# Performance work log

Hardware: AMD Instinct MI355X
Metric: run time of the kernel (lower is better)

## Reference

```python
import jax, jax.numpy as jnp
import numpy as np

D = 2048      # hidden_size
H = 16        # num_attention_heads
KVH = 4       # num_key_value_heads
HD = 128      # head_dim
E = 32        # num_experts
TOPK = 8      # num_experts_per_tok
F = 768       # moe_intermediate_size
EPS = 1e-6
THETA = 1000000.0
B, S = 2, 1024


def setup_inputs() -> dict:
    key = jax.random.key(0)
    ks = jax.random.split(key, 16)
    sc = lambda *shape: 1.0 / np.sqrt(shape[-2] if len(shape) > 1 else shape[0])
    return {
        "hidden_states": jax.random.normal(ks[0], (B, S, D), jnp.float32),
        "attention_mask": jnp.ones((B, S), jnp.bool_),
        "input_ln_scale": jnp.ones((D,), jnp.float32),
        "post_ln_scale": jnp.ones((D,), jnp.float32),
        "q_w": jax.random.normal(ks[1], (D, H * HD), jnp.float32) * sc(D, H * HD),
        "k_w": jax.random.normal(ks[2], (D, KVH * HD), jnp.float32) * sc(D, KVH * HD),
        "v_w": jax.random.normal(ks[3], (D, KVH * HD), jnp.float32) * sc(D, KVH * HD),
        "o_w": jax.random.normal(ks[4], (H * HD, D), jnp.float32) * sc(H * HD, D),
        "q_norm_scale": jnp.ones((HD,), jnp.float32),
        "k_norm_scale": jnp.ones((HD,), jnp.float32),
        "gate_w": jax.random.normal(ks[5], (D, E), jnp.float32) * sc(D, E),
        "gate_proj": jax.random.normal(ks[6], (E, D, F), jnp.float32) * sc(E, D, F),
        "up_proj": jax.random.normal(ks[7], (E, D, F), jnp.float32) * sc(E, D, F),
        "down_proj": jax.random.normal(ks[8], (E, F, D), jnp.float32) * sc(E, F, D),
    }


def _rms(x, scale):
    return x * jax.lax.rsqrt(jnp.mean(x * x, axis=-1, keepdims=True) + EPS) * scale


def _rope(x):
    # x: [B, S, h, HD]
    half = HD // 2
    inv_freq = 1.0 / (THETA ** (jnp.arange(0, half, dtype=jnp.float32) / half))
    freqs = jnp.arange(x.shape[1], dtype=jnp.float32)[:, None] * inv_freq  # [S, HD/2]
    cos = jnp.concatenate([jnp.cos(freqs)] * 2, axis=-1)[None, :, None, :]
    sin = jnp.concatenate([jnp.sin(freqs)] * 2, axis=-1)[None, :, None, :]
    rot = jnp.concatenate([-x[..., half:], x[..., :half]], axis=-1)
    return x * cos + rot * sin


def _forward(hidden_states, attention_mask, input_ln_scale, post_ln_scale,
             q_w, k_w, v_w, o_w, q_norm_scale, k_norm_scale,
             gate_w, gate_proj, up_proj, down_proj):
    b, s, _ = hidden_states.shape
    residual = hidden_states
    h = _rms(hidden_states, input_ln_scale)

    # ---- Qwen3 attention (GQA + per-head RMSNorm + RoPE, causal) ----
    q = _rms((h @ q_w).reshape(b, s, H, HD), q_norm_scale)
    k = _rms((h @ k_w).reshape(b, s, KVH, HD), k_norm_scale)
    v = (h @ v_w).reshape(b, s, KVH, HD)
    q, k = _rope(q), _rope(k)
    rep = H // KVH
    k = jnp.repeat(k, rep, axis=2)  # [B,S,H,HD]
    v = jnp.repeat(v, rep, axis=2)
    scores = jnp.einsum('bqhd,bkhd->bhqk', q, k) * (HD ** -0.5)
    causal = jnp.tril(jnp.ones((s, s), jnp.bool_))
    mask = causal[None, None] & attention_mask[:, None, None, :]
    scores = jnp.where(mask, scores, jnp.finfo(scores.dtype).min)
    attn = jax.nn.softmax(scores, axis=-1)
    ctx = jnp.einsum('bhqk,bkhd->bqhd', attn, v).reshape(b, s, H * HD)
    h = residual + ctx @ o_w

    # ---- MoE block ----
    residual = h
    x = _rms(h, post_ln_scale).reshape(-1, D)  # [N, D]
    router_logits = x @ gate_w                 # [N, E]
    routing_weights, selected = jax.lax.top_k(router_logits, k=TOPK)
    routing_weights = jax.nn.softmax(routing_weights, axis=-1)
    sel_flat = jnp.ravel(selected)                     # [N*K]
    x_exp = jnp.repeat(x, TOPK, axis=0)                # [N*K, D]
    sort_idx = jnp.argsort(sel_flat)
    unsort_idx = jnp.argsort(sort_idx)
    x_sorted = x_exp[sort_idx]
    group_sizes = jnp.bincount(sel_flat, length=E)
    gate_out = jax.lax.ragged_dot(x_sorted, gate_proj, group_sizes)
    up_out = jax.lax.ragged_dot(x_sorted, up_proj, group_sizes)
    activated = jax.nn.silu(gate_out) * up_out
    down_out = jax.lax.ragged_dot(activated, down_proj, group_sizes)
    unsorted = down_out[unsort_idx].reshape(-1, TOPK, D)
    moe_out = (unsorted * routing_weights[..., None]).sum(axis=1).reshape(b, s, D)
    return residual + moe_out


def reference(hidden_states, attention_mask, input_ln_scale, post_ln_scale,
              q_w, k_w, v_w, o_w, q_norm_scale, k_norm_scale,
              gate_w, gate_proj, up_proj, down_proj):
    return _forward(hidden_states, attention_mask, input_ln_scale, post_ln_scale,
                    q_w, k_w, v_w, o_w, q_norm_scale, k_norm_scale,
                    gate_w, gate_proj, up_proj, down_proj)
```

## Files before the change

### kernel.cpp

```cpp
#include <hip/hip_runtime.h>
#include <hip/hip_bf16.h>

#define D_ 2048
#define H_ 16
#define KVH_ 4
#define HD_ 128
#define E_ 32
#define TOPK_ 8
#define F_ 768
#define NB_ 2
#define SS_ 1024
#define NT_ 2048
#define NPAIR_ 16384

typedef __attribute__((ext_vector_type(8))) short short8;
typedef __attribute__((ext_vector_type(4))) float floatx4;
typedef __attribute__((ext_vector_type(4))) unsigned int uintx4;
typedef __attribute__((ext_vector_type(4))) unsigned short ushortx4;

__device__ __forceinline__ unsigned short f2bf(float f) {
  union { float f; unsigned u; } v; v.f = f;
  unsigned r = v.u + 0x7FFFu + ((v.u >> 16) & 1u);
  return (unsigned short)(r >> 16);
}
__device__ __forceinline__ float bf2f(unsigned short h) {
  union { unsigned u; float f; } v; v.u = ((unsigned)h) << 16;
  return v.f;
}
__device__ __forceinline__ void split2(float v, unsigned short& hi, unsigned short& lo) {
  unsigned short h = f2bf(v);
  hi = h;
  lo = f2bf(v - bf2f(h));
}
__device__ __forceinline__ void gload16(const unsigned short* g, unsigned short* l) {
  __builtin_amdgcn_global_load_lds(
      (const __attribute__((address_space(1))) unsigned int*)g,
      (__attribute__((address_space(3))) unsigned int*)l, 16, 0, 0);
}

__global__ __launch_bounds__(256) void tconv_kernel(const float* __restrict__ src,
                                                    unsigned short* __restrict__ dst,
                                                    int R, int C) {
  size_t off = (size_t)blockIdx.z * R * C;
  src += off; dst += off;
  __shared__ float t[32][33];
  int c0 = blockIdx.x * 32, r0 = blockIdx.y * 32;
  int row = threadIdx.x >> 3, c4 = (threadIdx.x & 7) * 4;
  float4 v = *(const float4*)(src + (size_t)(r0 + row) * C + c0 + c4);
  t[row][c4 + 0] = v.x; t[row][c4 + 1] = v.y; t[row][c4 + 2] = v.z; t[row][c4 + 3] = v.w;
  __syncthreads();
  ushortx4 o = { f2bf(t[c4 + 0][row]), f2bf(t[c4 + 1][row]),
                 f2bf(t[c4 + 2][row]), f2bf(t[c4 + 3][row]) };
  *(ushortx4*)(dst + (size_t)(c0 + row) * R + r0 + c4) = o;
}

__global__ __launch_bounds__(256) void tsplit_kernel(const float* __restrict__ src,
                                                     unsigned short* __restrict__ dhi,
                                                     unsigned short* __restrict__ dlo,
                                                     int R, int C) {
  __shared__ float t[32][33];
  int c0 = blockIdx.x * 32, r0 = blockIdx.y * 32;
  int row = threadIdx.x >> 3, c4 = (threadIdx.x & 7) * 4;
  float4 v = *(const float4*)(src + (size_t)(r0 + row) * C + c0 + c4);
  t[row][c4 + 0] = v.x; t[row][c4 + 1] = v.y; t[row][c4 + 2] = v.z; t[row][c4 + 3] = v.w;
  __syncthreads();
  ushortx4 oh, ol;
  #pragma unroll
  for (int i = 0; i < 4; ++i) {
    unsigned short hi, lo;
    split2(t[c4 + i][row], hi, lo);
    oh[i] = hi; ol[i] = lo;
  }
  size_t didx = (size_t)(c0 + row) * R + r0 + c4;
  *(ushortx4*)(dhi + didx) = oh;
  *(ushortx4*)(dlo + didx) = ol;
}

template<int MODE>
__global__ __launch_bounds__(256) void rms_kernel(const float* __restrict__ in,
                                                  const float* __restrict__ sc,
                                                  float* __restrict__ outf,
                                                  unsigned short* __restrict__ o1,
                                                  unsigned short* __restrict__ o2) {
  __shared__ float red[4];
  int row = blockIdx.x, tid = threadIdx.x;
  const float4* x4 = (const float4*)(in + (size_t)row * D_);
  float4 a = x4[tid], b = x4[tid + 256];
  float ss = a.x*a.x + a.y*a.y + a.z*a.z + a.w*a.w
           + b.x*b.x + b.y*b.y + b.z*b.z + b.w*b.w;
  #pragma unroll
  for (int off = 1; off < 64; off <<= 1) ss += __shfl_xor(ss, off);
  if ((tid & 63) == 0) red[tid >> 6] = ss;
  __syncthreads();
  float r = rsqrtf((red[0] + red[1] + red[2] + red[3]) * (1.0f / D_) + 1e-6f);
  const float4* s4 = (const float4*)sc;
  float4 sa = s4[tid], sb = s4[tid + 256];
  float va[8] = { a.x*r*sa.x, a.y*r*sa.y, a.z*r*sa.z, a.w*r*sa.w,
                  b.x*r*sb.x, b.y*r*sb.y, b.z*r*sb.z, b.w*r*sb.w };
  if (MODE == 0) {
    ushortx4 h0, l0, h1, l1;
    #pragma unroll
    for (int i = 0; i < 4; ++i) { unsigned short h, l; split2(va[i], h, l); h0[i] = h; l0[i] = l; }
    #pragma unroll
    for (int i = 0; i < 4; ++i) { unsigned short h, l; split2(va[4 + i], h, l); h1[i] = h; l1[i] = l; }
    *(ushortx4*)(o1 + (size_t)row * D_ + tid * 4) = h0;
    *(ushortx4*)(o2 + (size_t)row * D_ + tid * 4) = l0;
    *(ushortx4*)(o1 + (size_t)row * D_ + 1024 + tid * 4) = h1;
    *(ushortx4*)(o2 + (size_t)row * D_ + 1024 + tid * 4) = l1;
  } else {
    *(float4*)(outf + (size_t)row * D_ + tid * 4) = make_float4(va[0], va[1], va[2], va[3]);
    *(float4*)(outf + (size_t)row * D_ + 1024 + tid * 4) = make_float4(va[4], va[5], va[6], va[7]);
    ushortx4 h0 = { f2bf(va[0]), f2bf(va[1]), f2bf(va[2]), f2bf(va[3]) };
    ushortx4 h1 = { f2bf(va[4]), f2bf(va[5]), f2bf(va[6]), f2bf(va[7]) };
    *(ushortx4*)(o1 + (size_t)row * D_ + tid * 4) = h0;
    *(ushortx4*)(o1 + (size_t)row * D_ + 1024 + tid * 4) = h1;
  }
}

template<int EPI>
__global__ __launch_bounds__(256) void gemm_bb(const unsigned short* __restrict__ Ahi,
                                               const unsigned short* __restrict__ Alo,
                                               const unsigned short* __restrict__ Bhi,
                                               const unsigned short* __restrict__ Blo,
                                               const float* __restrict__ res,
                                               float* __restrict__ out,
                                               int M, int Nn, int K) {
  __shared__ unsigned short Ah[64 * 72], Al[64 * 72], Bh[64 * 72], Bl[64 * 72];
  int tid = threadIdx.x, l = tid & 63, wid = tid >> 6;
  int lr = l & 15, lk = (l >> 4) * 8;
  int m0 = blockIdx.y * 64, n0 = blockIdx.x * 64;
  int wr = (wid >> 1) * 32, wc = (wid & 1) * 32;
  int srow = tid >> 3, sch = (tid & 7) * 8;
  size_t aoff[2], boff[2];
  int loff[2];
  #pragma unroll
  for (int i = 0; i < 2; ++i) {
    aoff[i] = (size_t)(m0 + i * 32 + srow) * K + sch;
    boff[i] = (size_t)(n0 + i * 32 + srow) * K + sch;
    loff[i] = (i * 32 + srow) * 72 + sch;
  }
  floatx4 acc[2][2];
  #pragma unroll
  for (int i = 0; i < 2; ++i)
    #pragma unroll
    for (int j = 0; j < 2; ++j) acc[i][j] = (floatx4){0.f, 0.f, 0.f, 0.f};
  for (int k0 = 0; k0 < K; k0 += 64) {
    uintx4 vah[2], val[2], vbh[2], vbl[2];
    #pragma unroll
    for (int i = 0; i < 2; ++i) {
      vah[i] = *(const uintx4*)(Ahi + aoff[i] + k0);
      val[i] = *(const uintx4*)(Alo + aoff[i] + k0);
      vbh[i] = *(const uintx4*)(Bhi + boff[i] + k0);
      vbl[i] = *(const uintx4*)(Blo + boff[i] + k0);
    }
    __syncthreads();
    #pragma unroll
    for (int i = 0; i < 2; ++i) {
      *(uintx4*)&Ah[loff[i]] = vah[i];
      *(uintx4*)&Al[loff[i]] = val[i];
      *(uintx4*)&Bh[loff[i]] = vbh[i];
      *(uintx4*)&Bl[loff[i]] = vbl[i];
    }
    __syncthreads();
    #pragma unroll
    for (int ks = 0; ks < 2; ++ks) {
      short8 ah[2], al_[2], bh[2], bl_[2];
      #pragma unroll
      for (int i = 0; i < 2; ++i) {
        ah[i]  = *(const short8*)&Ah[(wr + i * 16 + lr) * 72 + ks * 32 + lk];
        al_[i] = *(const short8*)&Al[(wr + i * 16 + lr) * 72 + ks * 32 + lk];
        bh[i]  = *(const short8*)&Bh[(wc + i * 16 + lr) * 72 + ks * 32 + lk];
        bl_[i] = *(const short8*)&Bl[(wc + i * 16 + lr) * 72 + ks * 32 + lk];
      }
      #pragma unroll
      for (int i = 0; i < 2; ++i)
        #pragma unroll
        for (int j = 0; j < 2; ++j) {
          acc[i][j] = __builtin_amdgcn_mfma_f32_16x16x32_bf16(ah[i], bh[j], acc[i][j], 0, 0, 0);
          acc[i][j] = __builtin_amdgcn_mfma_f32_16x16x32_bf16(ah[i], bl_[j], acc[i][j], 0, 0, 0);
          acc[i][j] = __builtin_amdgcn_mfma_f32_16x16x32_bf16(al_[i], bh[j], acc[i][j], 0, 0, 0);
        }
    }
  }
  int rq = (l >> 4) * 4;
  #pragma unroll
  for (int i = 0; i < 2; ++i)
    #pragma unroll
    for (int j = 0; j < 2; ++j)
      #pragma unroll
      for (int r = 0; r < 4; ++r) {
        size_t idx = (size_t)(m0 + wr + i * 16 + rq + r) * Nn + (n0 + wc + j * 16 + lr);
        float v = acc[i][j][r];
        if (EPI == 1) v += res[idx];
        out[idx] = v;
      }
}

template<int EPI>
__global__ __launch_bounds__(256) void gemm_bb128g(const unsigned short* __restrict__ Ahi,
                                                   const unsigned short* __restrict__ Alo,
                                                   const unsigned short* __restrict__ Bhi,
                                                   const unsigned short* __restrict__ Blo,
                                                   const float* __restrict__ res,
                                                   float* __restrict__ out,
                                                   int M, int Nn, int K) {
  int g = blockIdx.x;
  int nwg = gridDim.x;
  int per = nwg >> 3;
  int sw = (g & 7) * per + (g >> 3);
  int my = M >> 7;
  int xt = sw / my, yt = sw - xt * my;
  int m0 = yt * 128, n0 = xt * 128;
  __shared__ unsigned short Ah[2][128 * 32], Al[2][128 * 32];
  __shared__ unsigned short Bh[2][128 * 32], Bl[2][128 * 32];
  int tid = threadIdx.x, l = tid & 63, wid = tid >> 6;
  int lr = l & 15, lk = (l >> 4) * 8;
  int wr = (wid >> 1) * 64, wc = (wid & 1) * 64;
  int srl = l >> 2;
  int sch = ((l & 3) ^ (srl & 3)) * 8;
  size_t aoffs[2], boffs[2];
  int ldo[2];
  #pragma unroll
  for (int i = 0; i < 2; ++i) {
    int r = wid * 32 + i * 16 + srl;
    aoffs[i] = (size_t)(m0 + r) * K + sch;
    boffs[i] = (size_t)(n0 + r) * K + sch;
    ldo[i] = (wid * 32 + i * 16) * 32;
  }
  floatx4 acc[4][4];
  #pragma unroll
  for (int i = 0; i < 4; ++i)
    #pragma unroll
    for (int j = 0; j < 4; ++j) acc[i][j] = (floatx4){0.f, 0.f, 0.f, 0.f};

  auto stage = [&](int sel, int k0) {
    #pragma unroll
    for (int i = 0; i < 2; ++i) {
      gload16(Ahi + aoffs[i] + k0, &Ah[sel][ldo[i]]);
      gload16(Alo + aoffs[i] + k0, &Al[sel][ldo[i]]);
      gload16(Bhi + boffs[i] + k0, &Bh[sel][ldo[i]]);
      gload16(Blo + boffs[i] + k0, &Bl[sel][ldo[i]]);
    }
  };

  int rsw = ((l >> 4) ^ (lr & 3)) << 3;
  stage(0, 0);
  asm volatile("s_waitcnt vmcnt(0)" ::: "memory");
  __syncthreads();
  for (int k0 = 0; k0 < K; k0 += 32) {
    int cur = (k0 >> 5) & 1;
    if (k0 + 32 < K) stage(cur ^ 1, k0 + 32);
    short8 ah[4], al_[4];
    #pragma unroll
    for (int i = 0; i < 4; ++i) {
      int ao = (wr + i * 16 + lr) * 32 + rsw;
      ah[i]  = *(const short8*)&Ah[cur][ao];
      al_[i] = *(const short8*)&Al[cur][ao];
    }
    #pragma unroll
    for (int j = 0; j < 4; ++j) {
      int bo = (wc + j * 16 + lr) * 32 + rsw;
      short8 bh  = *(const short8*)&Bh[cur][bo];
      short8 bl_ = *(const short8*)&Bl[cur][bo];
      #pragma unroll
      for (int i = 0; i < 4; ++i) {
        acc[i][j] = __builtin_amdgcn_mfma_f32_16x16x32_bf16(ah[i], bh, acc[i][j], 0, 0, 0);
        acc[i][j] = __builtin_amdgcn_mfma_f32_16x16x32_bf16(ah[i], bl_, acc[i][j], 0, 0, 0);
        acc[i][j] = __builtin_amdgcn_mfma_f32_16x16x32_bf16(al_[i], bh, acc[i][j], 0, 0, 0);
      }
    }
    asm volatile("s_waitcnt vmcnt(0)" ::: "memory");
    __syncthreads();
  }
  int rq = (l >> 4) * 4;
  #pragma unroll
  for (int i = 0; i < 4; ++i)
    #pragma unroll
    for (int j = 0; j < 4; ++j)
      #pragma unroll
      for (int r = 0; r < 4; ++r) {
        size_t idx = (size_t)(m0 + wr + i * 16 + rq + r) * Nn + (n0 + wc + j * 16 + lr);
        float v = acc[i][j][r];
        if (EPI == 1) v += res[idx];
        out[idx] = v;
      }
}

__global__ __launch_bounds__(256) void qknorm_rope_kernel(const float* __restrict__ qb,
                                                          const float* __restrict__ kb,
                                                          const float* __restrict__ qs,
                                                          const float* __restrict__ ks,
                                                          unsigned short* __restrict__ qhi,
                                                          unsigned short* __restrict__ qlo,
                                                          unsigned short* __restrict__ khi,
                                                          unsigned short* __restrict__ klo) {
  int gw = blockIdx.x * 4 + (threadIdx.x >> 6);
  int l = threadIdx.x & 63;
  const float* ptr; const float* sc; unsigned short *dhi, *dlo; int t;
  size_t orow;
  if (gw < NT_ * H_) { ptr = qb + (size_t)gw * HD_; sc = qs; dhi = qhi; dlo = qlo; orow = (size_t)gw * HD_; t = gw >> 4; }
  else { int r = gw - NT_ * H_; ptr = kb + (size_t)r * HD_; sc = ks; dhi = khi; dlo = klo; orow = (size_t)r * HD_; t = r >> 2; }
  int pos = t & (SS_ - 1);
  float2 x = *(const float2*)(ptr + 2 * l);
  float p2 = x.x * x.x + x.y * x.y;
  #pragma unroll
  for (int off = 1; off < 64; off <<= 1) p2 += __shfl_xor(p2, off);
  float rms = rsqrtf(p2 * (1.0f / HD_) + 1e-6f);
  float nx = x.x * rms * sc[2 * l];
  float ny = x.y * rms * sc[2 * l + 1];
  int j0 = (2 * l) & 63;
  float ang0 = pos * __expf(-(float)j0 * (13.815510557964274f / 64.0f));
  float ang1 = pos * __expf(-(float)(j0 + 1) * (13.815510557964274f / 64.0f));
  float s0, c0, s1, c1;
  sincosf(ang0, &s0, &c0);
  sincosf(ang1, &s1, &c1);
  float ox = __shfl_xor(nx, 32);
  float oy = __shfl_xor(ny, 32);
  float r0, r1;
  if (l < 32) { r0 = nx * c0 - ox * s0; r1 = ny * c1 - oy * s1; }
  else        { r0 = nx * c0 + ox * s0; r1 = ny * c1 + oy * s1; }
  unsigned short h0, l0, h1, l1;
  split2(r0, h0, l0);
  split2(r1, h1, l1);
  *(unsigned*)(dhi + orow + 2 * l) = (unsigned)h0 | ((unsigned)h1 << 16);
  *(unsigned*)(dlo + orow + 2 * l) = (unsigned)l0 | ((unsigned)l1 << 16);
}

__global__ __launch_bounds__(256) void vsplit_kernel(const float* __restrict__ vbuf,
                                                     unsigned short* __restrict__ vthi,
                                                     unsigned short* __restrict__ vtlo) {
  int d0 = blockIdx.x * 32, s0 = blockIdx.y * 32, bk = blockIdx.z;
  int b = bk >> 2, kvh = bk & 3;
  __shared__ float t[32][33];
  int row = threadIdx.x >> 3, c4 = (threadIdx.x & 7) * 4;
  float4 v = *(const float4*)(vbuf + ((size_t)(b * SS_ + s0 + row) * KVH_ + kvh) * HD_ + d0 + c4);
  t[row][c4 + 0] = v.x; t[row][c4 + 1] = v.y; t[row][c4 + 2] = v.z; t[row][c4 + 3] = v.w;
  __syncthreads();
  ushortx4 oh, ol;
  #pragma unroll
  for (int i = 0; i < 4; ++i) {
    unsigned short hi, lo;
    split2(t[c4 + i][row], hi, lo);
    oh[i] = hi; ol[i] = lo;
  }
  size_t idx = ((size_t)(b * KVH_ + kvh) * HD_ + d0 + row) * SS_ + s0 + c4;
  *(ushortx4*)(vthi + idx) = oh;
  *(ushortx4*)(vtlo + idx) = ol;
}

__global__ __launch_bounds__(256) void attn_kernel(const unsigned short* __restrict__ qhi,
                                                   const unsigned short* __restrict__ qlo,
                                                   const unsigned short* __restrict__ khi,
                                                   const unsigned short* __restrict__ klo,
                                                   const unsigned short* __restrict__ vthi,
                                                   const unsigned short* __restrict__ vtlo,
                                                   unsigned short* __restrict__ ctx_hi,
                                                   unsigned short* __restrict__ ctx_lo) {
  int qt = blockIdx.x, h = blockIdx.y, b = blockIdx.z;
  int kvh = h >> 2;
  int tid = threadIdx.x, l = tid & 63, wid = tid >> 6;
  int lr = l & 15, lk = (l >> 4) * 8;
  __shared__ unsigned short Kh[2][32 * 128], Kl[2][32 * 128];
  __shared__ unsigned short Vh[2][128 * 32], Vl[2][128 * 32];
  __shared__ unsigned short Ph[64 * 40], Pl[64 * 40];
  int qt0 = qt * 64;

  size_t qrow = ((size_t)((b * SS_ + qt0 + wid * 16 + lr) * H_) + h) * HD_;
  short8 qfh[4], qfl[4];
  #pragma unroll
  for (int t = 0; t < 4; ++t) {
    qfh[t] = *(const short8*)(qhi + qrow + t * 32 + lk);
    qfl[t] = *(const short8*)(qlo + qrow + t * 32 + lk);
  }

  float m[4], sum[4];
  #pragma unroll
  for (int r = 0; r < 4; ++r) { m[r] = -__builtin_inff(); sum[r] = 0.f; }
  floatx4 o[8];
  #pragma unroll
  for (int cb = 0; cb < 8; ++cb) o[cb] = (floatx4){0.f, 0.f, 0.f, 0.f};

  size_t vbase = ((size_t)(b * KVH_ + kvh) * HD_) * SS_;
  int nt = 2 * qt + 2;

  auto stage = [&](int sel, int kt) {
    int k0 = kt * 32;
    #pragma unroll
    for (int i = 0; i < 2; ++i) {
      int r = wid * 8 + i * 4 + (l >> 4);
      int ch = (l & 15) ^ (r & 7);
      size_t gk = ((size_t)((b * SS_ + k0 + r) * KVH_) + kvh) * HD_ + ch * 8;
      gload16(khi + gk, &Kh[sel][(wid * 8 + i * 4) * 128]);
      gload16(klo + gk, &Kl[sel][(wid * 8 + i * 4) * 128]);
    }
    #pragma unroll
    for (int i = 0; i < 2; ++i) {
      int r = wid * 32 + i * 16 + (l >> 2);
      int ch = (l & 3) ^ (r & 3);
      size_t gv = vbase + (size_t)r * SS_ + k0 + ch * 8;
      gload16(vthi + gv, &Vh[sel][(wid * 32 + i * 16) * 32]);
      gload16(vtlo + gv, &Vl[sel][(wid * 32 + i * 16) * 32]);
    }
  };

  stage(0, 0);
  asm volatile("s_waitcnt vmcnt(0)" ::: "memory");
  __syncthreads();

  for (int kt = 0; kt < nt; ++kt) {
    int cur = kt & 1;
    if (kt + 1 < nt) stage(cur ^ 1, kt + 1);
    int k0 = kt * 32;
    float sv[2][4];
    #pragma unroll
    for (int kbk = 0; kbk < 2; ++kbk) {
      int kr = kbk * 16 + lr;
      floatx4 s = (floatx4){0.f, 0.f, 0.f, 0.f};
      #pragma unroll
      for (int t = 0; t < 4; ++t) {
        int co = kr * 128 + (((t * 4 + (l >> 4)) ^ (lr & 7)) << 3);
        short8 kfh = *(const short8*)&Kh[cur][co];
        short8 kfl = *(const short8*)&Kl[cur][co];
        s = __builtin_amdgcn_mfma_f32_16x16x32_bf16(qfh[t], kfh, s, 0, 0, 0);
        s = __builtin_amdgcn_mfma_f32_16x16x32_bf16(qfh[t], kfl, s, 0, 0, 0);
        s = __builtin_amdgcn_mfma_f32_16x16x32_bf16(qfl[t], kfh, s, 0, 0, 0);
      }
      int key = k0 + kr;
      #pragma unroll
      for (int r = 0; r < 4; ++r) {
        int q = qt0 + wid * 16 + (l >> 4) * 4 + r;
        float x = s[r] * 0.08838834764831845f;
        sv[kbk][r] = (key <= q) ? x : -1e30f;
      }
    }
    float f[4], p[2][4];
    #pragma unroll
    for (int r = 0; r < 4; ++r) {
      float tm = fmaxf(sv[0][r], sv[1][r]);
      tm = fmaxf(tm, __shfl_xor(tm, 1));
      tm = fmaxf(tm, __shfl_xor(tm, 2));
      tm = fmaxf(tm, __shfl_xor(tm, 4));
      tm = fmaxf(tm, __shfl_xor(tm, 8));
      float mn = fmaxf(m[r], tm);
      f[r] = __expf(m[r] - mn);
      m[r] = mn;
      float rs = 0.f;
      #pragma unroll
      for (int kbk = 0; kbk < 2; ++kbk) { p[kbk][r] = __expf(sv[kbk][r] - mn); rs += p[kbk][r]; }
      rs += __shfl_xor(rs, 1); rs += __shfl_xor(rs, 2);
      rs += __shfl_xor(rs, 4); rs += __shfl_xor(rs, 8);
      sum[r] = sum[r] * f[r] + rs;
    }
    #pragma unroll
    for (int kbk = 0; kbk < 2; ++kbk)
      #pragma unroll
      for (int r = 0; r < 4; ++r)
        split2(p[kbk][r],
               Ph[(wid * 16 + (l >> 4) * 4 + r) * 40 + kbk * 16 + lr],
               Pl[(wid * 16 + (l >> 4) * 4 + r) * 40 + kbk * 16 + lr]);
    #pragma unroll
    for (int cb = 0; cb < 8; ++cb)
      #pragma unroll
      for (int r = 0; r < 4; ++r) o[cb][r] = o[cb][r] * f[r];
    int pco = (wid * 16 + lr) * 40 + lk;
    short8 pah = *(const short8*)&Ph[pco];
    short8 pal = *(const short8*)&Pl[pco];
    #pragma unroll
    for (int cb = 0; cb < 8; ++cb) {
      int vo = (cb * 16 + lr) * 32 + (((l >> 4) ^ (lr & 3)) << 3);
      short8 vbh = *(const short8*)&Vh[cur][vo];
      short8 vbl = *(const short8*)&Vl[cur][vo];
      o[cb] = __builtin_amdgcn_mfma_f32_16x16x32_bf16(pah, vbh, o[cb], 0, 0, 0);
      o[cb] = __builtin_amdgcn_mfma_f32_16x16x32_bf16(pah, vbl, o[cb], 0, 0, 0);
      o[cb] = __builtin_amdgcn_mfma_f32_16x16x32_bf16(pal, vbh, o[cb], 0, 0, 0);
    }
    asm volatile("s_waitcnt vmcnt(0)" ::: "memory");
    __syncthreads();
  }
  #pragma unroll
  for (int cb = 0; cb < 8; ++cb)
    #pragma unroll
    for (int r = 0; r < 4; ++r) {
      int q = qt0 + wid * 16 + (l >> 4) * 4 + r;
      int d = cb * 16 + lr;
      float val = o[cb][r] / sum[r];
      unsigned short hi, lo;
      split2(val, hi, lo);
      size_t idx = ((size_t)(b * SS_ + q)) * (H_ * HD_) + h * HD_ + d;
      ctx_hi[idx] = hi;
      ctx_lo[idx] = lo;
    }
}

__global__ __launch_bounds__(256) void router_kernel(const float* __restrict__ x2,
                                                     const float* __restrict__ gw,
                                                     float* __restrict__ logits) {
  int t = blockIdx.x * 4 + (threadIdx.x >> 6);
  int l = threadIdx.x & 63;
  float acc[32];
  #pragma unroll
  for (int e = 0; e < 32; ++e) acc[e] = 0.f;
  for (int i = 0; i < 32; ++i) {
    int d = i * 64 + l;
    float xv = x2[(size_t)t * D_ + d];
    const float4* wr = (const float4*)(gw + (size_t)d * E_);
    #pragma unroll
    for (int j = 0; j < 8; ++j) {
      float4 wv = wr[j];
      acc[4 * j + 0] += xv * wv.x; acc[4 * j + 1] += xv * wv.y;
      acc[4 * j + 2] += xv * wv.z; acc[4 * j + 3] += xv * wv.w;
    }
  }
  #pragma unroll
  for (int e = 0; e < 32; ++e) {
    acc[e] += __shfl_xor(acc[e], 1);  acc[e] += __shfl_xor(acc[e], 2);
    acc[e] += __shfl_xor(acc[e], 4);  acc[e] += __shfl_xor(acc[e], 8);
    acc[e] += __shfl_xor(acc[e], 16); acc[e] += __shfl_xor(acc[e], 32);
  }
  if (l == 0) {
    #pragma unroll
    for (int e = 0; e < 32; ++e) logits[(size_t)t * E_ + e] = acc[e];
  }
}

__global__ void topk_kernel(const float* __restrict__ logits, int* __restrict__ sel,
                            float* __restrict__ wts, int* __restrict__ counts) {
  int t = blockIdx.x * blockDim.x + threadIdx.x;
  if (t >= NT_) return;
  float v[32];
  for (int e = 0; e < 32; ++e) v[e] = logits[(size_t)t * E_ + e];
  float val[8]; int idx[8];
  for (int k = 0; k < 8; ++k) {
    float best = -__builtin_inff(); int bi = 0;
    for (int e = 0; e < 32; ++e) if (v[e] > best) { best = v[e]; bi = e; }
    val[k] = best; idx[k] = bi; v[bi] = -__builtin_inff();
  }
  float mx = val[0], s = 0.f; float ex[8];
  for (int k = 0; k < 8; ++k) { ex[k] = expf(val[k] - mx); s += ex[k]; }
  float inv = 1.f / s;
  for (int k = 0; k < 8; ++k) {
    sel[t * 8 + k] = idx[k];
    wts[t * 8 + k] = ex[k] * inv;
    atomicAdd(&counts[idx[k]], 1);
  }
}

__global__ void scan_kernel(const int* __restrict__ counts, int* __restrict__ offs,
                            int* __restrict__ cursors) {
  if (threadIdx.x == 0) {
    int c = 0;
    for (int e = 0; e < E_; ++e) { offs[e] = c; cursors[e] = c; c += counts[e]; }
  }
}

__global__ void scatter_kernel(const int* __restrict__ sel, const float* __restrict__ wts,
                               int* __restrict__ cursors, int* __restrict__ pair_t,
                               float* __restrict__ pair_w, int* __restrict__ pos) {
  int g = blockIdx.x * blockDim.x + threadIdx.x;
  if (g >= NPAIR_) return;
  int e = sel[g];
  int p = atomicAdd(&cursors[e], 1);
  pair_t[p] = g >> 3;
  pair_w[p] = wts[g];
  pos[g] = p;
}

__global__ __launch_bounds__(256, 3) void gateup_kernel(const unsigned short* __restrict__ xbf,
                                                        const unsigned short* __restrict__ gT,
                                                        const unsigned short* __restrict__ uT,
                                                        const int* __restrict__ counts,
                                                        const int* __restrict__ offs,
                                                        const int* __restrict__ pair_t,
                                                        const float* __restrict__ pair_w,
                                                        unsigned short* __restrict__ act) {
  int g = blockIdx.x;
  int lg = (g & ~127) | (((g & 7) << 4) | ((g >> 3) & 15));
  int e = lg / 192;
  int rem = lg - e * 192;
  int xt = rem >> 4, yt = rem & 15;
  int cnt = counts[e];
  int r0 = yt * 128;
  if (r0 >= cnt) return;
  int base = offs[e];
  int n0 = xt * 64;
  const unsigned short* G = gT + (size_t)e * F_ * D_;
  const unsigned short* U = uT + (size_t)e * F_ * D_;
  __shared__ unsigned short As[3][128 * 32], Gs[3][64 * 32], Us[3][64 * 32];
  int tid = threadIdx.x, l = tid & 63, wid = tid >> 6;
  int lr = l & 15, lk16 = l >> 4;
  int srl = l >> 2;
  int sch = ((l & 3) ^ ((srl >> 1) & 3)) * 8;
  const unsigned short* asrc[2];
  #pragma unroll
  for (int i = 0; i < 2; ++i) {
    int rowt = wid * 32 + i * 16 + srl;
    int cr = r0 + rowt; if (cr > cnt - 1) cr = cnt - 1;
    asrc[i] = xbf + (size_t)pair_t[base + cr] * D_ + sch;
  }
  const unsigned short* gsrc = G + (size_t)(n0 + wid * 16 + srl) * D_ + sch;
  const unsigned short* usrc = U + (size_t)(n0 + wid * 16 + srl) * D_ + sch;
  int wm = wid >> 1;
  int wn = wid & 1;
  floatx4 ag[4][2], au[4][2];
  #pragma unroll
  for (int i = 0; i < 4; ++i)
    #pragma unroll
    for (int j = 0; j < 2; ++j) { ag[i][j] = (floatx4){0.f,0.f,0.f,0.f}; au[i][j] = (floatx4){0.f,0.f,0.f,0.f}; }

  auto stage = [&](int sel, int kofs) {
    gload16(asrc[0] + kofs, &As[sel][(wid * 32) * 32]);
    gload16(asrc[1] + kofs, &As[sel][(wid * 32 + 16) * 32]);
    gload16(gsrc + kofs, &Gs[sel][(wid * 16) * 32]);
    gload16(usrc + kofs, &Us[sel][(wid * 16) * 32]);
  };

  const int nt = D_ / 32;
  stage(0, 0);
  stage(1, 32);
  for (int t = 0; t < nt; ++t) {
    int cur = t % 3;
    if (t + 1 < nt) { asm volatile("s_waitcnt vmcnt(4)" ::: "memory"); }
    else            { asm volatile("s_waitcnt vmcnt(0)" ::: "memory"); }
    __builtin_amdgcn_sched_barrier(0);
    __syncthreads();
    if (t + 2 < nt) stage((t + 2) % 3, (t + 2) * 32);
    int co = (lk16 ^ ((lr >> 1) & 3)) << 3;
    short8 a[4], gg[2], uu[2];
    #pragma unroll
    for (int i = 0; i < 4; ++i)
      a[i] = *(const short8*)&As[cur][(wm * 64 + i * 16 + lr) * 32 + co];
    #pragma unroll
    for (int j = 0; j < 2; ++j) {
      gg[j] = *(const short8*)&Gs[cur][(wn * 32 + j * 16 + lr) * 32 + co];
      uu[j] = *(const short8*)&Us[cur][(wn * 32 + j * 16 + lr) * 32 + co];
    }
    __builtin_amdgcn_s_setprio(1);
    #pragma unroll
    for (int i = 0; i < 4; ++i)
      #pragma unroll
      for (int j = 0; j < 2; ++j) {
        ag[i][j] = __builtin_amdgcn_mfma_f32_16x16x32_bf16(a[i], gg[j], ag[i][j], 0, 0, 0);
        au[i][j] = __builtin_amdgcn_mfma_f32_16x16x32_bf16(a[i], uu[j], au[i][j], 0, 0, 0);
      }
    __builtin_amdgcn_s_setprio(0);
  }
  int rq = (l >> 4) * 4;
  #pragma unroll
  for (int i = 0; i < 4; ++i)
    #pragma unroll
    for (int r = 0; r < 4; ++r) {
      int rowl = wm * 64 + i * 16 + rq + r;
      if (r0 + rowl < cnt) {
        int p = base + r0 + rowl;
        float pw = pair_w[p];
        size_t orow = (size_t)p * F_;
        #pragma unroll
        for (int j = 0; j < 2; ++j) {
          float gv = ag[i][j][r], uv = au[i][j][r];
          float a = (gv / (1.f + __expf(-gv))) * uv * pw;
          act[orow + n0 + wn * 32 + j * 16 + lr] = f2bf(a);
        }
      }
    }
}

__global__ __launch_bounds__(256, 3) void down_kernel(const unsigned short* __restrict__ act,
                                                      const unsigned short* __restrict__ dT,
                                                      const int* __restrict__ counts,
                                                      const int* __restrict__ offs,
                                                      unsigned short* __restrict__ dpre) {
  int g = blockIdx.x;
  int lg = (g & ~255) | (((g & 7) << 5) | ((g >> 3) & 31));
  int e = lg >> 8;
  int rem = lg & 255;
  int xt = rem >> 4, yt = rem & 15;
  int cnt = counts[e];
  int r0 = yt * 128;
  if (r0 >= cnt) return;
  int base = offs[e];
  int n0 = xt * 128;
  const unsigned short* B = dT + (size_t)e * ((size_t)D_ * F_);
  __shared__ unsigned short As[3][128 * 32], Bs[3][128 * 32];
  int tid = threadIdx.x, l = tid & 63, wid = tid >> 6;
  int lr = l & 15, lk16 = l >> 4;
  int srl = l >> 2;
  int sch = ((l & 3) ^ ((srl >> 1) & 3)) * 8;
  const unsigned short* asrc[2];
  const unsigned short* bsrc[2];
  #pragma unroll
  for (int i = 0; i < 2; ++i) {
    int rowt = wid * 32 + i * 16 + srl;
    int cr = r0 + rowt; if (cr > cnt - 1) cr = cnt - 1;
    asrc[i] = act + (size_t)(base + cr) * F_ + sch;
    bsrc[i] = B + (size_t)(n0 + rowt) * F_ + sch;
  }
  int wm = wid >> 1;
  int wn = wid & 1;
  floatx4 acc[4][4];
  #pragma unroll
  for (int i = 0; i < 4; ++i)
    #pragma unroll
    for (int j = 0; j < 4; ++j) acc[i][j] = (floatx4){0.f, 0.f, 0.f, 0.f};

  auto stage = [&](int sel, int kofs) {
    gload16(asrc[0] + kofs, &As[sel][(wid * 32) * 32]);
    gload16(asrc[1] + kofs, &As[sel][(wid * 32 + 16) * 32]);
    gload16(bsrc[0] + kofs, &Bs[sel][(wid * 32) * 32]);
    gload16(bsrc[1] + kofs, &Bs[sel][(wid * 32 + 16) * 32]);
  };

  const int nt = F_ / 32;
  stage(0, 0);
  stage(1, 32);
  for (int t = 0; t < nt; ++t) {
    int cur = t % 3;
    if (t + 1 < nt) { asm volatile("s_waitcnt vmcnt(4)" ::: "memory"); }
    else            { asm volatile("s_waitcnt vmcnt(0)" ::: "memory"); }
    __builtin_amdgcn_sched_barrier(0);
    __syncthreads();
    if (t + 2 < nt) stage((t + 2) % 3, (t + 2) * 32);
    int co = (lk16 ^ ((lr >> 1) & 3)) << 3;
    short8 a[4], b_[4];
    #pragma unroll
    for (int i = 0; i < 4; ++i) {
      a[i]  = *(const short8*)&As[cur][(wm * 64 + i * 16 + lr) * 32 + co];
      b_[i] = *(const short8*)&Bs[cur][(wn * 64 + i * 16 + lr) * 32 + co];
    }
    __builtin_amdgcn_s_setprio(1);
    #pragma unroll
    for (int i = 0; i < 4; ++i)
      #pragma unroll
      for (int j = 0; j < 4; ++j)
        acc[i][j] = __builtin_amdgcn_mfma_f32_16x16x32_bf16(a[i], b_[j], acc[i][j], 0, 0, 0);
    __builtin_amdgcn_s_setprio(0);
  }
  int rq = (l >> 4) * 4;
  #pragma unroll
  for (int i = 0; i < 4; ++i)
    #pragma unroll
    for (int r = 0; r < 4; ++r) {
      int rowl = wm * 64 + i * 16 + rq + r;
      if (r0 + rowl < cnt) {
        size_t orow = (size_t)(base + r0 + rowl) * D_;
        #pragma unroll
        for (int j = 0; j < 4; ++j)
          dpre[orow + n0 + wn * 64 + j * 16 + lr] = f2bf(acc[i][j][r]);
      }
    }
}

__global__ __launch_bounds__(256) void moe_gather_kernel(const unsigned short* __restrict__ dpre,
                                                         const int* __restrict__ pos,
                                                         float* __restrict__ out) {
  int t = blockIdx.x;
  int tid = threadIdx.x;
  int p[8];
  #pragma unroll
  for (int k = 0; k < 8; ++k) p[k] = pos[t * 8 + k];
  size_t orow = (size_t)t * D_;
  int col = tid * 8;
  float s[8];
  float4 o0 = *(const float4*)(out + orow + col);
  float4 o1 = *(const float4*)(out + orow + col + 4);
  s[0] = o0.x; s[1] = o0.y; s[2] = o0.z; s[3] = o0.w;
  s[4] = o1.x; s[5] = o1.y; s[6] = o1.z; s[7] = o1.w;
  #pragma unroll
  for (int k = 0; k < 8; ++k) {
    short8 v = *(const short8*)(dpre + (size_t)p[k] * D_ + col);
    #pragma unroll
    for (int j = 0; j < 8; ++j) s[j] += bf2f((unsigned short)v[j]);
  }
  *(float4*)(out + orow + col) = make_float4(s[0], s[1], s[2], s[3]);
  *(float4*)(out + orow + col + 4) = make_float4(s[4], s[5], s[6], s[7]);
}

extern "C" void kernel_launch(void* const* d_in, const int* in_sizes, int n_in,
                              void* d_out, int out_size, void* d_ws, size_t ws_size,
                              hipStream_t stream) {
  const float* hidden  = (const float*)d_in[0];
  const float* in_ln   = (const float*)d_in[2];
  const float* post_ln = (const float*)d_in[3];
  const float* q_w     = (const float*)d_in[4];
  const float* k_w     = (const float*)d_in[5];
  const float* v_w     = (const float*)d_in[6];
  const float* o_w     = (const float*)d_in[7];
  const float* q_ns    = (const float*)d_in[8];
  const float* k_ns    = (const float*)d_in[9];
  const float* gate_w  = (const float*)d_in[10];
  const float* gate_p  = (const float*)d_in[11];
  const float* up_p    = (const float*)d_in[12];
  const float* down_p  = (const float*)d_in[13];
  float* out = (float*)d_out;

  char* w = (char*)d_ws;
  size_t off = 0;
  auto alloc = [&](size_t b) { char* p = w + off; off += (b + 255) & ~(size_t)255; return p; };
  unsigned short* qThi = (unsigned short*)alloc((size_t)2048 * 2048 * 2);
  unsigned short* qTlo = (unsigned short*)alloc((size_t)2048 * 2048 * 2);
  unsigned short* kThi = (unsigned short*)alloc((size_t)512 * 2048 * 2);
  unsigned short* kTlo = (unsigned short*)alloc((size_t)512 * 2048 * 2);
  unsigned short* vThi = (unsigned short*)alloc((size_t)512 * 2048 * 2);
  unsigned short* vTlo = (unsigned short*)alloc((size_t)512 * 2048 * 2);
  unsigned short* oThi = (unsigned short*)alloc((size_t)2048 * 2048 * 2);
  unsigned short* oTlo = (unsigned short*)alloc((size_t)2048 * 2048 * 2);
  unsigned short* gT   = (unsigned short*)alloc((size_t)E_ * F_ * D_ * 2);
  unsigned short* uT   = (unsigned short*)alloc((size_t)E_ * F_ * D_ * 2);
  unsigned short* dT   = (unsigned short*)alloc((size_t)E_ * D_ * F_ * 2);
  unsigned short* h_hi = (unsigned short*)alloc((size_t)NT_ * D_ * 2);
  unsigned short* h_lo = (unsigned short*)alloc((size_t)NT_ * D_ * 2);
  float* qbuf  = (float*)alloc((size_t)NT_ * H_ * HD_ * 4);
  float* kbuf  = (float*)alloc((size_t)NT_ * KVH_ * HD_ * 4);
  float* vbuf  = (float*)alloc((size_t)NT_ * KVH_ * HD_ * 4);
  unsigned short* qhi = (unsigned short*)alloc((size_t)NT_ * H_ * HD_ * 2);
  unsigned short* qlo = (unsigned short*)alloc((size_t)NT_ * H_ * HD_ * 2);
  unsigned short* khi = (unsigned short*)alloc((size_t)NT_ * KVH_ * HD_ * 2);
  unsigned short* klo = (unsigned short*)alloc((size_t)NT_ * KVH_ * HD_ * 2);
  unsigned short* vthi = (unsigned short*)alloc((size_t)NT_ * KVH_ * HD_ * 2);
  unsigned short* vtlo = (unsigned short*)alloc((size_t)NT_ * KVH_ * HD_ * 2);
  unsigned short* ctx_hi = (unsigned short*)alloc((size_t)NT_ * H_ * HD_ * 2);
  unsigned short* ctx_lo = (unsigned short*)alloc((size_t)NT_ * H_ * HD_ * 2);
  float* x2    = (float*)alloc((size_t)NT_ * D_ * 4);
  unsigned short* x2bf = (unsigned short*)alloc((size_t)NT_ * D_ * 2);
  float* logits = (float*)alloc((size_t)NT_ * E_ * 4);
  int*   sel    = (int*)alloc((size_t)NT_ * TOPK_ * 4);
  float* wts    = (float*)alloc((size_t)NT_ * TOPK_ * 4);
  int*   counts = (int*)alloc(E_ * 4);
  int*   offs   = (int*)alloc(E_ * 4);
  int*   curs   = (int*)alloc(E_ * 4);
  int*   pair_t = (int*)alloc((size_t)NPAIR_ * 4);
  float* pair_w = (float*)alloc((size_t)NPAIR_ * 4);
  int*   pos    = (int*)alloc((size_t)NPAIR_ * 4);
  unsigned short* act = (unsigned short*)alloc((size_t)NPAIR_ * F_ * 2);
  unsigned short* dpre = (unsigned short*)alloc((size_t)NPAIR_ * D_ * 2);

  tsplit_kernel<<<dim3(64, 64), 256, 0, stream>>>(q_w, qThi, qTlo, 2048, 2048);
  tsplit_kernel<<<dim3(16, 64), 256, 0, stream>>>(k_w, kThi, kTlo, 2048, 512);
  tsplit_kernel<<<dim3(16, 64), 256, 0, stream>>>(v_w, vThi, vTlo, 2048, 512);
  tsplit_kernel<<<dim3(64, 64), 256, 0, stream>>>(o_w, oThi, oTlo, 2048, 2048);
  tconv_kernel<<<dim3(24, 64, 32), 256, 0, stream>>>(gate_p, gT, 2048, 768);
  tconv_kernel<<<dim3(24, 64, 32), 256, 0, stream>>>(up_p, uT, 2048, 768);
  tconv_kernel<<<dim3(64, 24, 32), 256, 0, stream>>>(down_p, dT, 768, 2048);

  rms_kernel<0><<<NT_, 256, 0, stream>>>(hidden, in_ln, nullptr, h_hi, h_lo);
  gemm_bb128g<0><<<256, 256, 0, stream>>>(h_hi, h_lo, qThi, qTlo, nullptr, qbuf, NT_, 2048, 2048);
  gemm_bb<0><<<dim3(8, 32), 256, 0, stream>>>(h_hi, h_lo, kThi, kTlo, nullptr, kbuf, NT_, 512, 2048);
  gemm_bb<0><<<dim3(8, 32), 256, 0, stream>>>(h_hi, h_lo, vThi, vTlo, nullptr, vbuf, NT_, 512, 2048);
  qknorm_rope_kernel<<<(NT_ * (H_ + KVH_)) / 4, 256, 0, stream>>>(qbuf, kbuf, q_ns, k_ns,
                                                                  qhi, qlo, khi, klo);
  vsplit_kernel<<<dim3(HD_ / 32, SS_ / 32, NB_ * KVH_), 256, 0, stream>>>(vbuf, vthi, vtlo);
  attn_kernel<<<dim3(SS_ / 64, H_, NB_), 256, 0, stream>>>(qhi, qlo, khi, klo, vthi, vtlo,
                                                           ctx_hi, ctx_lo);
  gemm_bb128g<1><<<256, 256, 0, stream>>>(ctx_hi, ctx_lo, oThi, oTlo, hidden, out, NT_, 2048, 2048);
  rms_kernel<1><<<NT_, 256, 0, stream>>>(out, post_ln, x2, x2bf, nullptr);
  (void)hipMemsetAsync(counts, 0, E_ * 4, stream);
  router_kernel<<<NT_ / 4, 256, 0, stream>>>(x2, gate_w, logits);
  topk_kernel<<<NT_ / 256, 256, 0, stream>>>(logits, sel, wts, counts);
  scan_kernel<<<1, 64, 0, stream>>>(counts, offs, curs);
  scatter_kernel<<<NPAIR_ / 256, 256, 0, stream>>>(sel, wts, curs, pair_t, pair_w, pos);
  gateup_kernel<<<192 * 32, 256, 0, stream>>>(x2bf, gT, uT, counts, offs, pair_t, pair_w, act);
  down_kernel<<<256 * 32, 256, 0, stream>>>(act, dT, counts, offs, dpre);
  moe_gather_kernel<<<NT_, 256, 0, stream>>>(dpre, pos, out);
}
```

Measured before the change: 1.024 ms.

## Unify projection GEMMs into a 128x64-tile kernel with single-barrier pipelining

Replaces the two projection GEMM kernels with one kernel using 128x64 output tiles. The grid doubles for the Q and O projections, and the K and V projections move from the 64x64 LDS-register kernel to the async-load double-buffered path. The loop now waits and syncs once per k-step before issuing the next stage, uses a new LDS swizzle, raises wave priority around the MFMA block, and sets a launch bound of 3 blocks. The aim is better occupancy and CU fill on the 256-CU part. The risk is less data reuse per tile.

```diff
diff --git a/kernel.cpp b/kernel.cpp
--- a/kernel.cpp
+++ b/kernel.cpp
@@ -118,168 +118,85 @@
 }
 
 template<int EPI>
-__global__ __launch_bounds__(256) void gemm_bb(const unsigned short* __restrict__ Ahi,
-                                               const unsigned short* __restrict__ Alo,
-                                               const unsigned short* __restrict__ Bhi,
-                                               const unsigned short* __restrict__ Blo,
-                                               const float* __restrict__ res,
-                                               float* __restrict__ out,
-                                               int M, int Nn, int K) {
-  __shared__ unsigned short Ah[64 * 72], Al[64 * 72], Bh[64 * 72], Bl[64 * 72];
-  int tid = threadIdx.x, l = tid & 63, wid = tid >> 6;
-  int lr = l & 15, lk = (l >> 4) * 8;
-  int m0 = blockIdx.y * 64, n0 = blockIdx.x * 64;
-  int wr = (wid >> 1) * 32, wc = (wid & 1) * 32;
-  int srow = tid >> 3, sch = (tid & 7) * 8;
-  size_t aoff[2], boff[2];
-  int loff[2];
-  #pragma unroll
-  for (int i = 0; i < 2; ++i) {
-    aoff[i] = (size_t)(m0 + i * 32 + srow) * K + sch;
-    boff[i] = (size_t)(n0 + i * 32 + srow) * K + sch;
-    loff[i] = (i * 32 + srow) * 72 + sch;
-  }
-  floatx4 acc[2][2];
-  #pragma unroll
-  for (int i = 0; i < 2; ++i)
-    #pragma unroll
-    for (int j = 0; j < 2; ++j) acc[i][j] = (floatx4){0.f, 0.f, 0.f, 0.f};
-  for (int k0 = 0; k0 < K; k0 += 64) {
-    uintx4 vah[2], val[2], vbh[2], vbl[2];
-    #pragma unroll
-    for (int i = 0; i < 2; ++i) {
-      vah[i] = *(const uintx4*)(Ahi + aoff[i] + k0);
-      val[i] = *(const uintx4*)(Alo + aoff[i] + k0);
-      vbh[i] = *(const uintx4*)(Bhi + boff[i] + k0);
-      vbl[i] = *(const uintx4*)(Blo + boff[i] + k0);
-    }
-    __syncthreads();
-    #pragma unroll
-    for (int i = 0; i < 2; ++i) {
-      *(uintx4*)&Ah[loff[i]] = vah[i];
-      *(uintx4*)&Al[loff[i]] = val[i];
-      *(uintx4*)&Bh[loff[i]] = vbh[i];
-      *(uintx4*)&Bl[loff[i]] = vbl[i];
-    }
-    __syncthreads();
-    #pragma unroll
-    for (int ks = 0; ks < 2; ++ks) {
-      short8 ah[2], al_[2], bh[2], bl_[2];
-      #pragma unroll
-      for (int i = 0; i < 2; ++i) {
-        ah[i]  = *(const short8*)&Ah[(wr + i * 16 + lr) * 72 + ks * 32 + lk];
-        al_[i] = *(const short8*)&Al[(wr + i * 16 + lr) * 72 + ks * 32 + lk];
-        bh[i]  = *(const short8*)&Bh[(wc + i * 16 + lr) * 72 + ks * 32 + lk];
-        bl_[i] = *(const short8*)&Bl[(wc + i * 16 + lr) * 72 + ks * 32 + lk];
-      }
-      #pragma unroll
-      for (int i = 0; i < 2; ++i)
-        #pragma unroll
-        for (int j = 0; j < 2; ++j) {
-          acc[i][j] = __builtin_amdgcn_mfma_f32_16x16x32_bf16(ah[i], bh[j], acc[i][j], 0, 0, 0);
-          acc[i][j] = __builtin_amdgcn_mfma_f32_16x16x32_bf16(ah[i], bl_[j], acc[i][j], 0, 0, 0);
-          acc[i][j] = __builtin_amdgcn_mfma_f32_16x16x32_bf16(al_[i], bh[j], acc[i][j], 0, 0, 0);
-        }
-    }
-  }
-  int rq = (l >> 4) * 4;
-  #pragma unroll
-  for (int i = 0; i < 2; ++i)
-    #pragma unroll
-    for (int j = 0; j < 2; ++j)
-      #pragma unroll
-      for (int r = 0; r < 4; ++r) {
-        size_t idx = (size_t)(m0 + wr + i * 16 + rq + r) * Nn + (n0 + wc + j * 16 + lr);
-        float v = acc[i][j][r];
-        if (EPI == 1) v += res[idx];
-        out[idx] = v;
-      }
-}
-
-template<int EPI>
-__global__ __launch_bounds__(256) void gemm_bb128g(const unsigned short* __restrict__ Ahi,
-                                                   const unsigned short* __restrict__ Alo,
-                                                   const unsigned short* __restrict__ Bhi,
-                                                   const unsigned short* __restrict__ Blo,
-                                                   const float* __restrict__ res,
-                                                   float* __restrict__ out,
-                                                   int M, int Nn, int K) {
+__global__ __launch_bounds__(256, 3) void gemm_pj(const unsigned short* __restrict__ Ahi,
+                                                  const unsigned short* __restrict__ Alo,
+                                                  const unsigned short* __restrict__ Bhi,
+                                                  const unsigned short* __restrict__ Blo,
+                                                  const float* __restrict__ res,
+                                                  float* __restrict__ out,
+                                                  int M, int Nn, int K) {
   int g = blockIdx.x;
   int nwg = gridDim.x;
   int per = nwg >> 3;
   int sw = (g & 7) * per + (g >> 3);
   int my = M >> 7;
   int xt = sw / my, yt = sw - xt * my;
-  int m0 = yt * 128, n0 = xt * 128;
+  int m0 = yt * 128, n0 = xt * 64;
   __shared__ unsigned short Ah[2][128 * 32], Al[2][128 * 32];
-  __shared__ unsigned short Bh[2][128 * 32], Bl[2][128 * 32];
+  __shared__ unsigned short Bh[2][64 * 32], Bl[2][64 * 32];
   int tid = threadIdx.x, l = tid & 63, wid = tid >> 6;
-  int lr = l & 15, lk = (l >> 4) * 8;
-  int wr = (wid >> 1) * 64, wc = (wid & 1) * 64;
+  int lr = l & 15, lk16 = l >> 4;
   int srl = l >> 2;
-  int sch = ((l & 3) ^ (srl & 3)) * 8;
-  size_t aoffs[2], boffs[2];
-  int ldo[2];
-  #pragma unroll
-  for (int i = 0; i < 2; ++i) {
-    int r = wid * 32 + i * 16 + srl;
-    aoffs[i] = (size_t)(m0 + r) * K + sch;
-    boffs[i] = (size_t)(n0 + r) * K + sch;
-    ldo[i] = (wid * 32 + i * 16) * 32;
-  }
-  floatx4 acc[4][4];
+  int sch = ((l & 3) ^ ((srl >> 1) & 3)) * 8;
+  size_t a0 = (size_t)(m0 + wid * 32 + srl) * K + sch;
+  size_t a1 = (size_t)(m0 + wid * 32 + 16 + srl) * K + sch;
+  size_t b0 = (size_t)(n0 + wid * 16 + srl) * K + sch;
+  int wm = wid >> 1;
+  int wn = wid & 1;
+  floatx4 acc[4][2];
   #pragma unroll
   for (int i = 0; i < 4; ++i)
     #pragma unroll
-    for (int j = 0; j < 4; ++j) acc[i][j] = (floatx4){0.f, 0.f, 0.f, 0.f};
+    for (int j = 0; j < 2; ++j) acc[i][j] = (floatx4){0.f, 0.f, 0.f, 0.f};
 
   auto stage = [&](int sel, int k0) {
-    #pragma unroll
-    for (int i = 0; i < 2; ++i) {
-      gload16(Ahi + aoffs[i] + k0, &Ah[sel][ldo[i]]);
-      gload16(Alo + aoffs[i] + k0, &Al[sel][ldo[i]]);
-      gload16(Bhi + boffs[i] + k0, &Bh[sel][ldo[i]]);
-      gload16(Blo + boffs[i] + k0, &Bl[sel][ldo[i]]);
-    }
+    gload16(Ahi + a0 + k0, &Ah[sel][(wid * 32) * 32]);
+    gload16(Ahi + a1 + k0, &Ah[sel][(wid * 32 + 16) * 32]);
+    gload16(Alo + a0 + k0, &Al[sel][(wid * 32) * 32]);
+    gload16(Alo + a1 + k0, &Al[sel][(wid * 32 + 16) * 32]);
+    gload16(Bhi + b0 + k0, &Bh[sel][(wid * 16) * 32]);
+    gload16(Blo + b0 + k0, &Bl[sel][(wid * 16) * 32]);
   };
 
-  int rsw = ((l >> 4) ^ (lr & 3)) << 3;
+  const int nt = K >> 5;
   stage(0, 0);
-  asm volatile("s_waitcnt vmcnt(0)" ::: "memory");
-  __syncthreads();
-  for (int k0 = 0; k0 < K; k0 += 32) {
-    int cur = (k0 >> 5) & 1;
-    if (k0 + 32 < K) stage(cur ^ 1, k0 + 32);
-    short8 ah[4], al_[4];
+  for (int t = 0; t < nt; ++t) {
+    int cur = t & 1;
+    asm volatile("s_waitcnt vmcnt(0)" ::: "memory");
+    __builtin_amdgcn_sched_barrier(0);
+    __syncthreads();
+    if (t + 1 < nt) stage(cur ^ 1, (t + 1) * 32);
+    int co = (lk16 ^ ((lr >> 1) & 3)) << 3;
+    short8 ah[4], al_[4], bh[2], bl_[2];
     #pragma unroll
     for (int i = 0; i < 4; ++i) {
-      int ao = (wr + i * 16 + lr) * 32 + rsw;
-      ah[i]  = *(const short8*)&Ah[cur][ao];
-      al_[i] = *(const short8*)&Al[cur][ao];
-    }
-    #pragma unroll
-    for (int j = 0; j < 4; ++j) {
-      int bo = (wc + j * 16 + lr) * 32 + rsw;
-      short8 bh  = *(const short8*)&Bh[cur][bo];
-      short8 bl_ = *(const short8*)&Bl[cur][bo];
-      #pragma unroll
-      for (int i = 0; i < 4; ++i) {
-        acc[i][j] = __builtin_amdgcn_mfma_f32_16x16x32_bf16(ah[i], bh, acc[i][j], 0, 0, 0);
-        acc[i][j] = __builtin_amdgcn_mfma_f32_16x16x32_bf16(ah[i], bl_, acc[i][j], 0, 0, 0);
-        acc[i][j] = __builtin_amdgcn_mfma_f32_16x16x32_bf16(al_[i], bh, acc[i][j], 0, 0, 0);
+      ah[i]  = *(const short8*)&Ah[cur][(wm * 64 + i * 16 + lr) * 32 + co];
+      al_[i] = *(const short8*)&Al[cur][(wm * 64 + i * 16 + lr) * 32 + co];
+    }
+    #pragma unroll
+    for (int j = 0; j < 2; ++j) {
+      bh[j]  = *(const short8*)&Bh[cur][(wn * 32 + j * 16 + lr) * 32 + co];
+      bl_[j] = *(const short8*)&Bl[cur][(wn * 32 + j * 16 + lr) * 32 + co];
+    }
+    __builtin_amdgcn_s_setprio(1);
+    #pragma unroll
+    for (int i = 0; i < 4; ++i)
+      #pragma unroll
+      for (int j = 0; j < 2; ++j) {
+        acc[i][j] = __builtin_amdgcn_mfma_f32_16x16x32_bf16(ah[i], bh[j], acc[i][j], 0, 0, 0);
+        acc[i][j] = __builtin_amdgcn_mfma_f32_16x16x32_bf16(ah[i], bl_[j], acc[i][j], 0, 0, 0);
+        acc[i][j] = __builtin_amdgcn_mfma_f32_16x16x32_bf16(al_[i], bh[j], acc[i][j], 0, 0, 0);
       }
-    }
-    asm volatile("s_waitcnt vmcnt(0)" ::: "memory");
-    __syncthreads();
+    __builtin_amdgcn_s_setprio(0);
   }
   int rq = (l >> 4) * 4;
   #pragma unroll
   for (int i = 0; i < 4; ++i)
     #pragma unroll
-    for (int j = 0; j < 4; ++j)
+    for (int j = 0; j < 2; ++j)
       #pragma unroll
       for (int r = 0; r < 4; ++r) {
-        size_t idx = (size_t)(m0 + wr + i * 16 + rq + r) * Nn + (n0 + wc + j * 16 + lr);
+        size_t idx = (size_t)(m0 + wm * 64 + i * 16 + rq + r) * Nn + (n0 + wn * 32 + j * 16 + lr);
         float v = acc[i][j][r];
         if (EPI == 1) v += res[idx];
         out[idx] = v;
@@ -842,15 +759,15 @@
   tconv_kernel<<<dim3(64, 24, 32), 256, 0, stream>>>(down_p, dT, 768, 2048);
 
   rms_kernel<0><<<NT_, 256, 0, stream>>>(hidden, in_ln, nullptr, h_hi, h_lo);
-  gemm_bb128g<0><<<256, 256, 0, stream>>>(h_hi, h_lo, qThi, qTlo, nullptr, qbuf, NT_, 2048, 2048);
-  gemm_bb<0><<<dim3(8, 32), 256, 0, stream>>>(h_hi, h_lo, kThi, kTlo, nullptr, kbuf, NT_, 512, 2048);
-  gemm_bb<0><<<dim3(8, 32), 256, 0, stream>>>(h_hi, h_lo, vThi, vTlo, nullptr, vbuf, NT_, 512, 2048);
+  gemm_pj<0><<<512, 256, 0, stream>>>(h_hi, h_lo, qThi, qTlo, nullptr, qbuf, NT_, 2048, 2048);
+  gemm_pj<0><<<128, 256, 0, stream>>>(h_hi, h_lo, kThi, kTlo, nullptr, kbuf, NT_, 512, 2048);
+  gemm_pj<0><<<128, 256, 0, stream>>>(h_hi, h_lo, vThi, vTlo, nullptr, vbuf, NT_, 512, 2048);
   qknorm_rope_kernel<<<(NT_ * (H_ + KVH_)) / 4, 256, 0, stream>>>(qbuf, kbuf, q_ns, k_ns,
                                                                   qhi, qlo, khi, klo);
   vsplit_kernel<<<dim3(HD_ / 32, SS_ / 32, NB_ * KVH_), 256, 0, stream>>>(vbuf, vthi, vtlo);
   attn_kernel<<<dim3(SS_ / 64, H_, NB_), 256, 0, stream>>>(qhi, qlo, khi, klo, vthi, vtlo,
                                                            ctx_hi, ctx_lo);
-  gemm_bb128g<1><<<256, 256, 0, stream>>>(ctx_hi, ctx_lo, oThi, oTlo, hidden, out, NT_, 2048, 2048);
+  gemm_pj<1><<<512, 256, 0, stream>>>(ctx_hi, ctx_lo, oThi, oTlo, hidden, out, NT_, 2048, 2048);
   rms_kernel<1><<<NT_, 256, 0, stream>>>(out, post_ln, x2, x2bf, nullptr);
   (void)hipMemsetAsync(counts, 0, E_ * 4, stream);
   router_kernel<<<NT_ / 4, 256, 0, stream>>>(x2, gate_w, logits);
```

After: 1.039 ms. No clear change (+1.4%).
